# Optimization experiments

Measured on AMD Instinct MI355X. Metric: run time of the kernel, lower is better.

The kernel has to match this reference:

```python
import jax, jax.numpy as jnp
import numpy as np

ALPHA = 0.2  # LeakyReLU negative slope
MASK_FILL = -9e15


def setup_inputs() -> dict:
    key = jax.random.key(0)
    k_x, k_adj, k_W, k_a = jax.random.split(key, 4)
    B, N, Fin, T, O = 8, 1024, 64, 8, 128
    x = jax.random.normal(k_x, (B, N, Fin, T), dtype=jnp.float32)
    adj = (jax.random.uniform(k_adj, (N, N)) < 0.05).astype(jnp.float32)
    adj = jnp.maximum(adj, jnp.eye(N, dtype=jnp.float32))
    W = jax.random.normal(k_W, (Fin, O), dtype=jnp.float32) * (1.414 * (6.0 / (Fin + O)) ** 0.5)
    a = jax.random.normal(k_a, (2 * O, 1), dtype=jnp.float32) * (1.414 * (6.0 / (2 * O + 1)) ** 0.5)
    return {"x": x, "adj": adj, "W": W, "a": a}


def reference(x, adj, W, a):
    # x: (B, N, Fin, T), adj: (N, N), W: (Fin, O), a: (2O, 1)
    O = W.shape[1]
    xt = jnp.transpose(x, (0, 3, 1, 2))                 # (B, T, N, Fin)
    Wh = jnp.einsum('btnf,fo->btno', xt, W)             # (B, T, N, O)
    a1 = a[:O, 0]                                       # (O,)
    a2 = a[O:, 0]                                       # (O,)
    Wh1 = Wh @ a1                                       # (B, T, N)
    Wh2 = Wh @ a2                                       # (B, T, N)
    e = Wh1[..., :, None] + Wh2[..., None, :]           # (B, T, N, N): e_ij = Wh1_i + Wh2_j
    e = jax.nn.leaky_relu(e, negative_slope=ALPHA)
    e = jnp.where(adj > 0, e, MASK_FILL)
    attn = jax.nn.softmax(e, axis=-1)                   # softmax over neighbors j (torch dim=1 on (N,N))
    # dropout on attention is identity at inference (training=False)
    h_prime = jnp.einsum('btij,btjo->btio', attn, Wh)   # (B, T, N, O)
    out = jnp.transpose(h_prime, (0, 2, 3, 1))          # (B, N, O, T)
    return jax.nn.elu(out)                              # concat=True -> ELU
```

## Files before the change

kernel.cpp:

```cpp
#include <hip/hip_runtime.h>
#include <math.h>
#include <stdint.h>

#define ALPHA 0.2f

typedef __attribute__((ext_vector_type(8)))  short bf16x8;
typedef __attribute__((ext_vector_type(4)))  float f32x4;
typedef __attribute__((ext_vector_type(16))) float f32x16;

__device__ __forceinline__ uint32_t pack_bf16(float a, float b) {
    return ((__float_as_uint(a) + 0x8000u) >> 16) |
           ((__float_as_uint(b) + 0x8000u) & 0xFFFF0000u);
}

__global__ __launch_bounds__(512) void k_wh(const float* __restrict__ x,
                                            const float* __restrict__ W,
                                            const float* __restrict__ a,
                                            uint4* __restrict__ Whf,
                                            float* __restrict__ Wh1,
                                            float* __restrict__ Wh2) {
    __shared__ float xs[16 * 512];
    __shared__ float Wv[128 * 68];

    const int tid = threadIdx.x;
    const int b   = blockIdx.x & 7;
    const int jt  = blockIdx.x >> 3;

    const float4* xg4 = (const float4*)(x + (size_t)(b * 1024 + jt * 16) * 512);
    #pragma unroll
    for (int i = 0; i < 4; ++i) {
        int    idx = tid + i * 512;
        float4 v   = xg4[idx];
        int jl  = idx >> 7;
        int rem = idx & 127;
        int f   = rem >> 1;
        int tq  = rem & 1;
        int kk  = f ^ ((jl >> 2) << 2);
        float* dst = &xs[jl * 512 + (tq * 4) * 64 + kk];
        dst[0]   = v.x;
        dst[64]  = v.y;
        dst[128] = v.z;
        dst[192] = v.w;
    }
    const float4* Wg4 = (const float4*)W;
    #pragma unroll
    for (int i = 0; i < 4; ++i) {
        int    idx = tid + i * 512;
        float4 v   = Wg4[idx];
        int k  = idx >> 5;
        int o0 = (idx & 31) * 4;
        #pragma unroll
        for (int c = 0; c < 4; ++c) {
            int o   = o0 + c;
            int adr = o * 68 + ((((k >> 2) ^ ((o >> 3) & 7)) << 2) | (k & 3));
            Wv[adr] = (&v.x)[c];
        }
    }
    __syncthreads();

    const int w  = tid >> 6;
    const int l  = tid & 63;
    const int q  = l >> 4;
    const int om = l & 15;
    const int t  = w;

    float acc[4][8];
    #pragma unroll
    for (int jj = 0; jj < 4; ++jj)
        #pragma unroll
        for (int nt = 0; nt < 8; ++nt) acc[jj][nt] = 0.f;

    for (int kc = 0; kc < 64; kc += 4) {
        float4 xv[4], wv[8];
        const int kx = kc ^ (q << 2);
        #pragma unroll
        for (int jj = 0; jj < 4; ++jj)
            xv[jj] = *(const float4*)&xs[(q * 4 + jj) * 512 + t * 64 + kx];
        #pragma unroll
        for (int nt = 0; nt < 8; ++nt) {
            int og  = nt * 16 + om;
            int grp = (kc >> 2) ^ ((nt * 2 + (om >> 3)) & 7);
            wv[nt]  = *(const float4*)&Wv[og * 68 + grp * 4];
        }
        #pragma unroll
        for (int jj = 0; jj < 4; ++jj) {
            #pragma unroll
            for (int nt = 0; nt < 8; ++nt) {
                float s = acc[jj][nt];
                s = fmaf(xv[jj].x, wv[nt].x, s);
                s = fmaf(xv[jj].y, wv[nt].y, s);
                s = fmaf(xv[jj].z, wv[nt].z, s);
                s = fmaf(xv[jj].w, wv[nt].w, s);
                acc[jj][nt] = s;
            }
        }
    }

    const int bt = b * 8 + t;

    float a1v[8], a2v[8];
    #pragma unroll
    for (int nt = 0; nt < 8; ++nt) {
        a1v[nt] = a[nt * 16 + om];
        a2v[nt] = a[128 + nt * 16 + om];
    }
    #pragma unroll
    for (int jj = 0; jj < 4; ++jj) {
        float s1 = 0.f, s2 = 0.f;
        #pragma unroll
        for (int nt = 0; nt < 8; ++nt) {
            s1 = fmaf(acc[jj][nt], a1v[nt], s1);
            s2 = fmaf(acc[jj][nt], a2v[nt], s2);
        }
        #pragma unroll
        for (int off = 1; off < 16; off <<= 1) {
            s1 += __shfl_xor(s1, off);
            s2 += __shfl_xor(s2, off);
        }
        if (om == 0) {
            int j = jt * 16 + q * 4 + jj;
            Wh1[bt * 1024 + j] = s1;
            Wh2[bt * 1024 + j] = s2;
        }
    }

    #pragma unroll
    for (int nt = 0; nt < 8; ++nt) {
        uint2 st;
        st.x = pack_bf16(acc[0][nt], acc[1][nt]);
        st.y = pack_bf16(acc[2][nt], acc[3][nt]);
        int    lane2 = ((q >> 1) << 5) | ((nt & 1) << 4) | om;
        size_t fidx  = ((size_t)(bt * 4 + (nt >> 1)) * 64 + jt) * 64 + lane2;
        char*  p     = (char*)(Whf + fidx) + ((q & 1) << 3);
        *(uint2*)p = st;
    }
}

__global__ __launch_bounds__(256) void k_adjb(const float* __restrict__ adj,
                                              unsigned char* __restrict__ adjq) {
    int idx = blockIdx.x * 256 + threadIdx.x;
    int i   = idx >> 7;
    int pos = idx & 127;
    const float4* a4 = (const float4*)adj + idx * 2;
    float4 v0 = a4[0], v1 = a4[1];
    unsigned int by = 0;
    by |= (v0.x > 0.f) ? 1u : 0u;
    by |= (v0.y > 0.f) ? 2u : 0u;
    by |= (v0.z > 0.f) ? 4u : 0u;
    by |= (v0.w > 0.f) ? 8u : 0u;
    by |= (v1.x > 0.f) ? 16u : 0u;
    by |= (v1.y > 0.f) ? 32u : 0u;
    by |= (v1.z > 0.f) ? 64u : 0u;
    by |= (v1.w > 0.f) ? 128u : 0u;
    adjq[(i << 7) + ((pos & 1) << 6) + (((pos >> 1) & 1) << 5) + (pos >> 2)] = (unsigned char)by;
}

__global__ __launch_bounds__(256) void k_agg(const uint4* __restrict__ Whf,
                                             const float* __restrict__ Wh1,
                                             const float* __restrict__ Wh2,
                                             const unsigned char* __restrict__ adjq,
                                             float* __restrict__ out) {
    __shared__ __attribute__((aligned(16))) uint4 bstage[2][2048];
    __shared__ __attribute__((aligned(16))) float efsE[1024];
    __shared__ __attribute__((aligned(16))) float efsF[1024];
    __shared__ float wh1s[128];
    __shared__ float m2s[4];

    const int tid   = threadIdx.x;
    const int b     = blockIdx.x & 7;
    const int t     = (blockIdx.x >> 3) & 7;
    const int itile = blockIdx.x >> 6;
    const int bt    = b * 8 + t;
    const int i0    = itile * 128;

    const int w   = tid >> 6;
    const int l   = tid & 63;
    const int col = l & 31;
    const int g   = l >> 5;
    const int row = w * 32 + col;

    const uint4* plane = Whf + (size_t)bt * 16384;

    uint4 pf[8];
    #pragma unroll
    for (int f = 0; f < 8; ++f) pf[f] = plane[(w * 64 + f) * 64 + l];

    const uint4* ap = (const uint4*)(adjq + ((size_t)(i0 + row) << 7) + (g << 6));
    uint4 am[4];
    #pragma unroll
    for (int f = 0; f < 4; ++f) am[f] = ap[f];

    const float* wh2g = Wh2 + bt * 1024;
    float mx = -1e30f;
    #pragma unroll
    for (int rep = 0; rep < 4; ++rep) {
        int   j  = tid + rep * 256;
        float h2 = wh2g[j];
        efsE[j] = __expf(h2);
        efsF[j] = __expf(ALPHA * h2);
        mx = fmaxf(mx, h2);
    }
    #pragma unroll
    for (int off = 1; off < 64; off <<= 1) mx = fmaxf(mx, __shfl_xor(mx, off));
    if (l == 0) m2s[w] = mx;
    if (tid < 128) wh1s[tid] = Wh1[bt * 1024 + i0 + tid];

    #pragma unroll
    for (int f = 0; f < 8; ++f) bstage[0][(w * 8 + f) * 64 + l] = pf[f];
    __syncthreads();

    const float M2 = fmaxf(fmaxf(m2s[0], m2s[1]), fmaxf(m2s[2], m2s[3]));
    const float h1 = wh1s[row];
    const float e0 = h1 + M2;
    const float mp = fmaxf(e0, ALPHA * e0);
    const float Af = __expf(h1 - mp);
    const float Bf = __expf(ALPHA * h1 - mp);

    f32x16 acc[4];
    #pragma unroll
    for (int nt2 = 0; nt2 < 4; ++nt2)
        #pragma unroll
        for (int r = 0; r < 16; ++r) acc[nt2][r] = 0.f;
    f32x16 accl;
    #pragma unroll
    for (int r = 0; r < 16; ++r) accl[r] = 0.f;

    bf16x8 ones;
    #pragma unroll
    for (int i = 0; i < 8; ++i) ones[i] = (short)0x3F80;

    #pragma unroll
    for (int u = 0; u < 8; ++u) {
        if (u + 1 < 8) {
            #pragma unroll
            for (int f = 0; f < 8; ++f)
                pf[f] = plane[(w * 64 + (u + 1) * 8 + f) * 64 + l];
        }

        #pragma unroll
        for (int ts = 0; ts < 8; ++ts) {
            const int jb = u * 128 + ts * 16 + g * 8;
            float4 E0 = *(const float4*)&efsE[jb];
            float4 E1 = *(const float4*)&efsE[jb + 4];
            float4 F0 = *(const float4*)&efsF[jb];
            float4 F1 = *(const float4*)&efsF[jb + 4];

            const int      pe = (ts & 1) * 32 + u * 4 + (ts >> 1);
            const uint4    av = am[pe >> 4];
            const int      cc = (pe >> 2) & 3;
            const uint32_t cw = (cc == 0) ? av.x : (cc == 1) ? av.y
                               : (cc == 2) ? av.z : av.w;
            const uint32_t by = (cw >> ((pe & 3) * 8)) & 0xFFu;

            float p[8];
            p[0] = fmaxf(Af * E0.x, Bf * F0.x) * (float)((by >> 0) & 1u);
            p[1] = fmaxf(Af * E0.y, Bf * F0.y) * (float)((by >> 1) & 1u);
            p[2] = fmaxf(Af * E0.z, Bf * F0.z) * (float)((by >> 2) & 1u);
            p[3] = fmaxf(Af * E0.w, Bf * F0.w) * (float)((by >> 3) & 1u);
            p[4] = fmaxf(Af * E1.x, Bf * F1.x) * (float)((by >> 4) & 1u);
            p[5] = fmaxf(Af * E1.y, Bf * F1.y) * (float)((by >> 5) & 1u);
            p[6] = fmaxf(Af * E1.z, Bf * F1.z) * (float)((by >> 6) & 1u);
            p[7] = fmaxf(Af * E1.w, Bf * F1.w) * (float)((by >> 7) & 1u);

            union { uint32_t u32[4]; bf16x8 v; } pk;
            #pragma unroll
            for (int r = 0; r < 4; ++r)
                pk.u32[r] = pack_bf16(p[2 * r], p[2 * r + 1]);

            #pragma unroll
            for (int nt2 = 0; nt2 < 4; ++nt2) {
                union { uint4 u4; bf16x8 v; } br;
                br.u4 = bstage[u & 1][(nt2 * 8 + ts) * 64 + l];
                acc[nt2] = __builtin_amdgcn_mfma_f32_32x32x16_bf16(
                    pk.v, br.v, acc[nt2], 0, 0, 0);
            }
            accl = __builtin_amdgcn_mfma_f32_32x32x16_bf16(
                pk.v, ones, accl, 0, 0, 0);
        }

        if (u + 1 < 8) {
            #pragma unroll
            for (int f = 0; f < 8; ++f)
                bstage[(u + 1) & 1][(w * 8 + f) * 64 + l] = pf[f];
        }
        __syncthreads();
    }

    float* og = out + ((size_t)(b * 1024 + i0 + w * 32)) * 1024 + t;
    #pragma unroll
    for (int reg = 0; reg < 16; ++reg) {
        const int   r    = (reg & 3) + 8 * (reg >> 2) + 4 * g;
        const float linv = 1.0f / accl[reg];
        #pragma unroll
        for (int nt2 = 0; nt2 < 4; ++nt2) {
            float v = acc[nt2][reg] * linv;
            v = v > 0.f ? v : __expf(v) - 1.f;
            og[(size_t)r * 1024 + (nt2 * 32 + col) * 8] = v;
        }
    }
}

extern "C" void kernel_launch(void* const* d_in, const int* in_sizes, int n_in,
                              void* d_out, int out_size, void* d_ws, size_t ws_size,
                              hipStream_t stream) {
    const float* x   = (const float*)d_in[0];
    const float* adj = (const float*)d_in[1];
    const float* W   = (const float*)d_in[2];
    const float* a   = (const float*)d_in[3];
    float* out = (float*)d_out;

    uint4*         Whf  = (uint4*)d_ws;
    float*         Wh1  = (float*)(Whf + 1048576);
    float*         Wh2  = Wh1 + 65536;
    unsigned char* adjq = (unsigned char*)(Wh2 + 65536);

    k_wh  <<<512, 512, 0, stream>>>(x, W, a, Whf, Wh1, Wh2);
    k_adjb<<<512, 256, 0, stream>>>(adj, adjq);
    k_agg <<<512, 256, 0, stream>>>(Whf, Wh1, Wh2, adjq, out);
}
```

Baseline: 145.4 us.

## Merge adjacency packing into projection kernel and stream Wh fragments directly from global

```diff
diff --git a/kernel.cpp b/kernel.cpp
--- a/kernel.cpp
+++ b/kernel.cpp
@@ -5,7 +5,6 @@
 #define ALPHA 0.2f
 
 typedef __attribute__((ext_vector_type(8)))  short bf16x8;
-typedef __attribute__((ext_vector_type(4)))  float f32x4;
 typedef __attribute__((ext_vector_type(16))) float f32x16;
 
 __device__ __forceinline__ uint32_t pack_bf16(float a, float b) {
@@ -13,14 +12,36 @@
            ((__float_as_uint(b) + 0x8000u) & 0xFFFF0000u);
 }
 
-__global__ __launch_bounds__(512) void k_wh(const float* __restrict__ x,
-                                            const float* __restrict__ W,
-                                            const float* __restrict__ a,
-                                            uint4* __restrict__ Whf,
-                                            float* __restrict__ Wh1,
-                                            float* __restrict__ Wh2) {
+__global__ __launch_bounds__(512) void k_pre(const float* __restrict__ x,
+                                             const float* __restrict__ W,
+                                             const float* __restrict__ a,
+                                             const float* __restrict__ adj,
+                                             uint4* __restrict__ Whf,
+                                             float* __restrict__ Wh1,
+                                             float* __restrict__ Wh2,
+                                             unsigned char* __restrict__ adjq) {
     __shared__ float xs[16 * 512];
     __shared__ float Wv[128 * 68];
+
+    if (blockIdx.x >= 512) {
+        int idx = (blockIdx.x - 512) * 512 + threadIdx.x;
+        int i   = idx >> 7;
+        int pos = idx & 127;
+        const float4* a4 = (const float4*)adj + idx * 2;
+        float4 v0 = a4[0], v1 = a4[1];
+        unsigned int by = 0;
+        by |= (v0.x > 0.f) ? 1u : 0u;
+        by |= (v0.y > 0.f) ? 2u : 0u;
+        by |= (v0.z > 0.f) ? 4u : 0u;
+        by |= (v0.w > 0.f) ? 8u : 0u;
+        by |= (v1.x > 0.f) ? 16u : 0u;
+        by |= (v1.y > 0.f) ? 32u : 0u;
+        by |= (v1.z > 0.f) ? 64u : 0u;
+        by |= (v1.w > 0.f) ? 128u : 0u;
+        adjq[(i << 7) + ((pos & 1) << 6) + (((pos >> 1) & 1) << 5) + (pos >> 2)] =
+            (unsigned char)by;
+        return;
+    }
 
     const int tid = threadIdx.x;
     const int b   = blockIdx.x & 7;
@@ -136,31 +157,11 @@
     }
 }
 
-__global__ __launch_bounds__(256) void k_adjb(const float* __restrict__ adj,
-                                              unsigned char* __restrict__ adjq) {
-    int idx = blockIdx.x * 256 + threadIdx.x;
-    int i   = idx >> 7;
-    int pos = idx & 127;
-    const float4* a4 = (const float4*)adj + idx * 2;
-    float4 v0 = a4[0], v1 = a4[1];
-    unsigned int by = 0;
-    by |= (v0.x > 0.f) ? 1u : 0u;
-    by |= (v0.y > 0.f) ? 2u : 0u;
-    by |= (v0.z > 0.f) ? 4u : 0u;
-    by |= (v0.w > 0.f) ? 8u : 0u;
-    by |= (v1.x > 0.f) ? 16u : 0u;
-    by |= (v1.y > 0.f) ? 32u : 0u;
-    by |= (v1.z > 0.f) ? 64u : 0u;
-    by |= (v1.w > 0.f) ? 128u : 0u;
-    adjq[(i << 7) + ((pos & 1) << 6) + (((pos >> 1) & 1) << 5) + (pos >> 2)] = (unsigned char)by;
-}
-
-__global__ __launch_bounds__(256) void k_agg(const uint4* __restrict__ Whf,
-                                             const float* __restrict__ Wh1,
-                                             const float* __restrict__ Wh2,
-                                             const unsigned char* __restrict__ adjq,
-                                             float* __restrict__ out) {
-    __shared__ __attribute__((aligned(16))) uint4 bstage[2][2048];
+__global__ __launch_bounds__(256, 4) void k_agg(const uint4* __restrict__ Whf,
+                                                const float* __restrict__ Wh1,
+                                                const float* __restrict__ Wh2,
+                                                const unsigned char* __restrict__ adjq,
+                                                float* __restrict__ out) {
     __shared__ __attribute__((aligned(16))) float efsE[1024];
     __shared__ __attribute__((aligned(16))) float efsF[1024];
     __shared__ float wh1s[128];
@@ -181,10 +182,6 @@
 
     const uint4* plane = Whf + (size_t)bt * 16384;
 
-    uint4 pf[8];
-    #pragma unroll
-    for (int f = 0; f < 8; ++f) pf[f] = plane[(w * 64 + f) * 64 + l];
-
     const uint4* ap = (const uint4*)(adjq + ((size_t)(i0 + row) << 7) + (g << 6));
     uint4 am[4];
     #pragma unroll
@@ -204,9 +201,6 @@
     for (int off = 1; off < 64; off <<= 1) mx = fmaxf(mx, __shfl_xor(mx, off));
     if (l == 0) m2s[w] = mx;
     if (tid < 128) wh1s[tid] = Wh1[bt * 1024 + i0 + tid];
-
-    #pragma unroll
-    for (int f = 0; f < 8; ++f) bstage[0][(w * 8 + f) * 64 + l] = pf[f];
     __syncthreads();
 
     const float M2 = fmaxf(fmaxf(m2s[0], m2s[1]), fmaxf(m2s[2], m2s[3]));
@@ -221,29 +215,19 @@
     for (int nt2 = 0; nt2 < 4; ++nt2)
         #pragma unroll
         for (int r = 0; r < 16; ++r) acc[nt2][r] = 0.f;
-    f32x16 accl;
-    #pragma unroll
-    for (int r = 0; r < 16; ++r) accl[r] = 0.f;
-
-    bf16x8 ones;
-    #pragma unroll
-    for (int i = 0; i < 8; ++i) ones[i] = (short)0x3F80;
+    float sacc = 0.f;
 
     #pragma unroll
     for (int u = 0; u < 8; ++u) {
-        if (u + 1 < 8) {
-            #pragma unroll
-            for (int f = 0; f < 8; ++f)
-                pf[f] = plane[(w * 64 + (u + 1) * 8 + f) * 64 + l];
-        }
-
         #pragma unroll
         for (int ts = 0; ts < 8; ++ts) {
-            const int jb = u * 128 + ts * 16 + g * 8;
-            float4 E0 = *(const float4*)&efsE[jb];
-            float4 E1 = *(const float4*)&efsE[jb + 4];
-            float4 F0 = *(const float4*)&efsF[jb];
-            float4 F1 = *(const float4*)&efsF[jb + 4];
+            const int step = u * 8 + ts;
+
+            union { uint4 u4; bf16x8 v; } q0, q1, q2, q3;
+            q0.u4 = plane[(0 * 64 + step) * 64 + l];
+            q1.u4 = plane[(1 * 64 + step) * 64 + l];
+            q2.u4 = plane[(2 * 64 + step) * 64 + l];
+            q3.u4 = plane[(3 * 64 + step) * 64 + l];
 
             const int      pe = (ts & 1) * 32 + u * 4 + (ts >> 1);
             const uint4    av = am[pe >> 4];
@@ -252,45 +236,47 @@
                                : (cc == 2) ? av.z : av.w;
             const uint32_t by = (cw >> ((pe & 3) * 8)) & 0xFFu;
 
-            float p[8];
-            p[0] = fmaxf(Af * E0.x, Bf * F0.x) * (float)((by >> 0) & 1u);
-            p[1] = fmaxf(Af * E0.y, Bf * F0.y) * (float)((by >> 1) & 1u);
-            p[2] = fmaxf(Af * E0.z, Bf * F0.z) * (float)((by >> 2) & 1u);
-            p[3] = fmaxf(Af * E0.w, Bf * F0.w) * (float)((by >> 3) & 1u);
-            p[4] = fmaxf(Af * E1.x, Bf * F1.x) * (float)((by >> 4) & 1u);
-            p[5] = fmaxf(Af * E1.y, Bf * F1.y) * (float)((by >> 5) & 1u);
-            p[6] = fmaxf(Af * E1.z, Bf * F1.z) * (float)((by >> 6) & 1u);
-            p[7] = fmaxf(Af * E1.w, Bf * F1.w) * (float)((by >> 7) & 1u);
+            const int jb = u * 128 + ts * 16 + g * 8;
 
             union { uint32_t u32[4]; bf16x8 v; } pk;
-            #pragma unroll
-            for (int r = 0; r < 4; ++r)
-                pk.u32[r] = pack_bf16(p[2 * r], p[2 * r + 1]);
-
-            #pragma unroll
-            for (int nt2 = 0; nt2 < 4; ++nt2) {
-                union { uint4 u4; bf16x8 v; } br;
-                br.u4 = bstage[u & 1][(nt2 * 8 + ts) * 64 + l];
-                acc[nt2] = __builtin_amdgcn_mfma_f32_32x32x16_bf16(
-                    pk.v, br.v, acc[nt2], 0, 0, 0);
+
+            {
+                float4 E0 = *(const float4*)&efsE[jb];
+                float4 F0 = *(const float4*)&efsF[jb];
+                float p0 = fmaxf(Af * E0.x, Bf * F0.x) * (float)((by >> 0) & 1u);
+                float p1 = fmaxf(Af * E0.y, Bf * F0.y) * (float)((by >> 1) & 1u);
+                float p2 = fmaxf(Af * E0.z, Bf * F0.z) * (float)((by >> 2) & 1u);
+                float p3 = fmaxf(Af * E0.w, Bf * F0.w) * (float)((by >> 3) & 1u);
+                sacc += (p0 + p1) + (p2 + p3);
+                pk.u32[0] = pack_bf16(p0, p1);
+                pk.u32[1] = pack_bf16(p2, p3);
             }
-            accl = __builtin_amdgcn_mfma_f32_32x32x16_bf16(
-                pk.v, ones, accl, 0, 0, 0);
-        }
-
-        if (u + 1 < 8) {
-            #pragma unroll
-            for (int f = 0; f < 8; ++f)
-                bstage[(u + 1) & 1][(w * 8 + f) * 64 + l] = pf[f];
-        }
-        __syncthreads();
-    }
+            {
+                float4 E1 = *(const float4*)&efsE[jb + 4];
+                float4 F1 = *(const float4*)&efsF[jb + 4];
+                float p4 = fmaxf(Af * E1.x, Bf * F1.x) * (float)((by >> 4) & 1u);
+                float p5 = fmaxf(Af * E1.y, Bf * F1.y) * (float)((by >> 5) & 1u);
+                float p6 = fmaxf(Af * E1.z, Bf * F1.z) * (float)((by >> 6) & 1u);
+                float p7 = fmaxf(Af * E1.w, Bf * F1.w) * (float)((by >> 7) & 1u);
+                sacc += (p4 + p5) + (p6 + p7);
+                pk.u32[2] = pack_bf16(p4, p5);
+                pk.u32[3] = pack_bf16(p6, p7);
+            }
+
+            acc[0] = __builtin_amdgcn_mfma_f32_32x32x16_bf16(pk.v, q0.v, acc[0], 0, 0, 0);
+            acc[1] = __builtin_amdgcn_mfma_f32_32x32x16_bf16(pk.v, q1.v, acc[1], 0, 0, 0);
+            acc[2] = __builtin_amdgcn_mfma_f32_32x32x16_bf16(pk.v, q2.v, acc[2], 0, 0, 0);
+            acc[3] = __builtin_amdgcn_mfma_f32_32x32x16_bf16(pk.v, q3.v, acc[3], 0, 0, 0);
+        }
+    }
+
+    float tot = sacc + __shfl_xor(sacc, 32);
 
     float* og = out + ((size_t)(b * 1024 + i0 + w * 32)) * 1024 + t;
     #pragma unroll
     for (int reg = 0; reg < 16; ++reg) {
         const int   r    = (reg & 3) + 8 * (reg >> 2) + 4 * g;
-        const float linv = 1.0f / accl[reg];
+        const float linv = 1.0f / __shfl(tot, r);
         #pragma unroll
         for (int nt2 = 0; nt2 < 4; ++nt2) {
             float v = acc[nt2][reg] * linv;
@@ -314,7 +300,6 @@
     float*         Wh2  = Wh1 + 65536;
     unsigned char* adjq = (unsigned char*)(Wh2 + 65536);
 
-    k_wh  <<<512, 512, 0, stream>>>(x, W, a, Whf, Wh1, Wh2);
-    k_adjb<<<512, 256, 0, stream>>>(adj, adjq);
-    k_agg <<<512, 256, 0, stream>>>(Whf, Wh1, Wh2, adjq, out);
+    k_pre<<<768, 512, 0, stream>>>(x, W, a, adj, Whf, Wh1, Wh2, adjq);
+    k_agg<<<512, 256, 0, stream>>>(Whf, Wh1, Wh2, adjq, out);
 }
```

Measured after the change: 426.6 us. 193% more time.
